# Kernel optimization log

Measured on AMD Instinct MI355X. Metric: run time of the kernel, lower is better.

Reference implementation:

```python
import jax, jax.numpy as jnp
import numpy as np

DIM = 2560
N_HEAD = 32
HEAD_DIM = 80
ROT_DIM = 32  # head_dim * partial_rotary_factor
INTER = 10240
EPS = 1e-5
BASE = 10000.0


def setup_inputs() -> dict:
    key = jax.random.key(0)
    ks = jax.random.split(key, 12)
    B, S, D, I = 1, 2048, DIM, INTER
    s = lambda k, shape, scale: (jax.random.normal(k, shape, jnp.float32) * scale)
    return {
        "x": s(ks[0], (B, S, D), 1.0),
        "input_pos": jnp.arange(S, dtype=jnp.int32),
        "mask": jnp.tril(jnp.ones((S, S), dtype=bool)),
        "ln_w": jnp.ones((D,), jnp.float32),
        "ln_b": jnp.zeros((D,), jnp.float32),
        "wqkv_w": s(ks[1], (3 * D, D), 0.02),
        "wqkv_b": jnp.zeros((3 * D,), jnp.float32),
        "wo_w": s(ks[2], (D, D), 0.02),
        "wo_b": jnp.zeros((D,), jnp.float32),
        "w1_w": s(ks[3], (I, D), 0.02),
        "w1_b": jnp.zeros((I,), jnp.float32),
        "w2_w": s(ks[4], (D, I), 0.02),
        "w2_b": jnp.zeros((D,), jnp.float32),
    }


def _rope_cos_sin(positions):
    # positions: [S] int; returns cos,sin of shape [S, ROT_DIM]
    inv_freq = 1.0 / (BASE ** (jnp.arange(0, ROT_DIM, 2, dtype=jnp.float32) / ROT_DIM))
    freqs = positions.astype(jnp.float32)[:, None] * inv_freq[None, :]  # [S, ROT/2]
    emb = jnp.concatenate([freqs, freqs], axis=-1)  # [S, ROT]
    return jnp.cos(emb), jnp.sin(emb)


def _rotate_half(t):
    t1, t2 = jnp.split(t, 2, axis=-1)
    return jnp.concatenate([-t2, t1], axis=-1)


def _apply_rope(t, cos, sin):
    # t: [B,H,S,hd]; rotary applied to first ROT_DIM dims (partial rotary)
    t_rot, t_pass = t[..., :ROT_DIM], t[..., ROT_DIM:]
    t_rot = t_rot * cos[None, None] + _rotate_half(t_rot) * sin[None, None]
    return jnp.concatenate([t_rot, t_pass], axis=-1)


def reference(x, input_pos, mask, ln_w, ln_b, wqkv_w, wqkv_b, wo_w, wo_b,
              w1_w, w1_b, w2_w, w2_b):
    B, S, D = x.shape
    H, hd = N_HEAD, HEAD_DIM
    # shared LayerNorm (parallel block)
    mu = jnp.mean(x, axis=-1, keepdims=True)
    var = jnp.mean(jnp.square(x - mu), axis=-1, keepdims=True)
    h = (x - mu) * jax.lax.rsqrt(var + EPS) * ln_w + ln_b

    # fused QKV
    qkv = h @ wqkv_w.T + wqkv_b  # [B,S,3D]
    q, k, v = jnp.split(qkv, 3, axis=-1)
    q = q.reshape(B, S, H, hd).transpose(0, 2, 1, 3)  # [B,H,S,hd]
    k = k.reshape(B, S, H, hd).transpose(0, 2, 1, 3)
    v = v.reshape(B, S, H, hd).transpose(0, 2, 1, 3)

    cos, sin = _rope_cos_sin(input_pos)
    q = _apply_rope(q, cos, sin)
    k = _apply_rope(k, cos, sin)

    # causal attention
    scores = jnp.einsum("bhqd,bhkd->bhqk", q, k) / np.sqrt(hd).astype(np.float32)
    scores = jnp.where(mask[None, None], scores, jnp.float32(-1e9))
    attn = jax.nn.softmax(scores, axis=-1)
    y = jnp.einsum("bhqk,bhkd->bhqd", attn, v)  # [B,H,S,hd]
    y = y.transpose(0, 2, 1, 3).reshape(B, S, D)
    attn_out = y @ wo_w.T + wo_b

    # fused MLP (phi2: gelu_new / tanh approx)
    ffn = jax.nn.gelu(h @ w1_w.T + w1_b, approximate=True) @ w2_w.T + w2_b

    return attn_out + ffn + x
```

## Files before the change

kernel.cpp:

```cpp
#include <hip/hip_runtime.h>
#include <cstdint>

#define S_LEN 2048
#define DMODEL 2560
#define NHEADS 32
#define HDIM 80
#define DINTER 10240

typedef unsigned short u16;
typedef __bf16 bf16x8 __attribute__((ext_vector_type(8)));
typedef float f32x4 __attribute__((ext_vector_type(4)));

__device__ __forceinline__ float us2f(u16 u) {
  return __builtin_bit_cast(float, ((uint32_t)u) << 16);
}
__device__ __forceinline__ u16 f2us(float f) {
  uint32_t x = __builtin_bit_cast(uint32_t, f);
  x += 0x7fffu + ((x >> 16) & 1u);
  return (u16)(x >> 16);
}

typedef __attribute__((address_space(1))) void gas_void;
typedef __attribute__((address_space(3))) void las_void;
__device__ __forceinline__ void gld16(const void* g, void* l) {
  __builtin_amdgcn_global_load_lds((gas_void*)g, (las_void*)l, 16, 0, 0);
}

#define VMW(N) asm volatile("s_waitcnt vmcnt(" #N ")" ::: "memory")
#define BARRIER()                          \
  do {                                     \
    asm volatile("" ::: "memory");         \
    __builtin_amdgcn_s_barrier();          \
    asm volatile("" ::: "memory");         \
  } while (0)

__global__ void f2b_kernel(const float* __restrict__ src, u16* __restrict__ dst) {
  const size_t i = ((size_t)blockIdx.x * 256 + threadIdx.x) * 8;
  const float4 a = *(const float4*)(src + i);
  const float4 b = *(const float4*)(src + i + 4);
  u16 o[8] = {f2us(a.x), f2us(a.y), f2us(a.z), f2us(a.w),
              f2us(b.x), f2us(b.y), f2us(b.z), f2us(b.w)};
  *(uint4*)(dst + i) = *(uint4*)o;
}

__global__ void initout_kernel(const float* __restrict__ x,
                               const float* __restrict__ wo_b,
                               const float* __restrict__ w2_b,
                               float* __restrict__ out) {
  const size_t idx = ((size_t)blockIdx.x * 256 + threadIdx.x) * 4;
  const int c0 = (int)(idx % DMODEL);
  const float4 vx = *(const float4*)(x + idx);
  const float4 b1 = *(const float4*)(wo_b + c0);
  const float4 b2 = *(const float4*)(w2_b + c0);
  float4 vo;
  vo.x = vx.x + b1.x + b2.x;
  vo.y = vx.y + b1.y + b2.y;
  vo.z = vx.z + b1.z + b2.z;
  vo.w = vx.w + b1.w + b2.w;
  *(float4*)(out + idx) = vo;
}

__global__ void ln_kernel(const float* __restrict__ x, const float* __restrict__ w,
                          const float* __restrict__ b, u16* __restrict__ h) {
  const int s = blockIdx.x, tid = threadIdx.x;
  const float* xr = x + (size_t)s * DMODEL;
  float v[10];
  float sum = 0.f, sq = 0.f;
#pragma unroll
  for (int j = 0; j < 10; j++) {
    v[j] = xr[tid + j * 256];
    sum += v[j];
    sq += v[j] * v[j];
  }
#pragma unroll
  for (int o = 32; o > 0; o >>= 1) {
    sum += __shfl_down(sum, o, 64);
    sq += __shfl_down(sq, o, 64);
  }
  __shared__ float red[8];
  const int wave = tid >> 6, lane = tid & 63;
  if (lane == 0) { red[wave] = sum; red[4 + wave] = sq; }
  __syncthreads();
  sum = red[0] + red[1] + red[2] + red[3];
  sq = red[4] + red[5] + red[6] + red[7];
  const float mu = sum * (1.0f / DMODEL);
  const float var = sq * (1.0f / DMODEL) - mu * mu;
  const float rstd = rsqrtf(var + 1e-5f);
  u16* hr = h + (size_t)s * DMODEL;
#pragma unroll
  for (int j = 0; j < 10; j++) {
    const int d = tid + j * 256;
    hr[d] = f2us((v[j] - mu) * rstd * w[d] + b[d]);
  }
}

template <int ACT, int MODE>
__launch_bounds__(512, 2)
__global__ void gemm256(const u16* __restrict__ A, const u16* __restrict__ B,
                        const float* __restrict__ bias, void* __restrict__ Cv,
                        int M, int N, int K) {
  __shared__ __align__(16) u16 lds[4][16384];
  const int tid = threadIdx.x;
  const int w = tid >> 6, lane = tid & 63;
  const int quad = lane >> 4, l15 = lane & 15;
  const int wm = w >> 2, wn = w & 3;

  const int nwg = gridDim.x * gridDim.y;
  const int flat = blockIdx.x + gridDim.x * blockIdx.y;
  const int swz = (flat & 7) * (nwg >> 3) + (flat >> 3);
  const int ntN = N >> 8;
  const int bm = swz / ntN, bn = swz % ntN;

  const int Kc = K / gridDim.z;
  const int k0 = Kc * blockIdx.z;
  const int nt = Kc >> 6;

  const int stgCol = (((lane & 7) ^ ((lane >> 3) & 7)) * 8);
  const u16* Ag = A + ((size_t)bm * 256 + w * 8 + (lane >> 3)) * K + k0 + stgCol;
  const u16* Bg = B + ((size_t)bn * 256 + w * 8 + (lane >> 3)) * K + k0 + stgCol;

  const int q8 = quad * 8;
  const int swz3 = (l15 & 7) * 8;
  const int arow = wm * 64 + l15;
  const int brow = wn * 32 + l15;

#define STG_HALF(MAT, GP, BUF, HF, KT)                                       \
  do {                                                                       \
    gld16((GP) + (size_t)((HF) * 128) * K + (size_t)(KT) * 64,               \
          &lds[(BUF) * 2 + (MAT)][(HF) * 8192 + w * 512]);                   \
    gld16((GP) + (size_t)((HF) * 128 + 64) * K + (size_t)(KT) * 64,          \
          &lds[(BUF) * 2 + (MAT)][(HF) * 8192 + 4096 + w * 512]);            \
  } while (0)

#define LDS_A(DST, BUF, MH)                                                  \
  _Pragma("unroll") for (int mf_ = 0; mf_ < 4; mf_++)                        \
  _Pragma("unroll") for (int kk_ = 0; kk_ < 2; kk_++)                        \
      DST[mf_][kk_] = *(const bf16x8*)&lds[(BUF) * 2]                        \
          [(arow + (MH) * 128 + mf_ * 16) * 64 + ((kk_ * 32 + q8) ^ swz3)];

#define LDS_B(DST, BUF, NH)                                                  \
  _Pragma("unroll") for (int nf_ = 0; nf_ < 2; nf_++)                        \
  _Pragma("unroll") for (int kk_ = 0; kk_ < 2; kk_++)                        \
      DST[nf_][kk_] = *(const bf16x8*)&lds[(BUF) * 2 + 1]                    \
          [(brow + (NH) * 128 + nf_ * 16) * 64 + ((kk_ * 32 + q8) ^ swz3)];

#define MFMA_C(MH, NH, AF, BF)                                               \
  do {                                                                       \
    __builtin_amdgcn_s_setprio(1);                                           \
    _Pragma("unroll") for (int kk_ = 0; kk_ < 2; kk_++)                      \
    _Pragma("unroll") for (int mf_ = 0; mf_ < 4; mf_++)                      \
    _Pragma("unroll") for (int nf_ = 0; nf_ < 2; nf_++)                      \
        acc[(MH) * 4 + mf_][(NH) * 2 + nf_] =                                \
            __builtin_amdgcn_mfma_f32_16x16x32_bf16(                         \
                AF[mf_][kk_], BF[nf_][kk_],                                  \
                acc[(MH) * 4 + mf_][(NH) * 2 + nf_], 0, 0, 0);               \
    __builtin_amdgcn_s_setprio(0);                                           \
  } while (0)

  f32x4 acc[8][4] = {};
  bf16x8 aH0[4][2], aH1[4][2], bH0[2][2], bH1[2][2];

  STG_HALF(0, Ag, 0, 0, 0);
  STG_HALF(1, Bg, 0, 0, 0);
  STG_HALF(1, Bg, 0, 1, 0);
  STG_HALF(0, Ag, 0, 1, 0);
  VMW(4);
  BARRIER();
  LDS_A(aH0, 0, 0);
  LDS_B(bH0, 0, 0);

  for (int t = 0; t < nt; ++t) {
    const int bc = t & 1, ob = bc ^ 1;
    const bool more = (t + 1 < nt);
    VMW(0);
    BARRIER();
    if (more) {
      STG_HALF(0, Ag, ob, 0, t + 1);
      STG_HALF(1, Bg, ob, 0, t + 1);
    }
    LDS_B(bH1, bc, 1);
    MFMA_C(0, 0, aH0, bH0);
    if (more) STG_HALF(1, Bg, ob, 1, t + 1);
    LDS_A(aH1, bc, 1);
    MFMA_C(0, 1, aH0, bH1);
    if (more) STG_HALF(0, Ag, ob, 1, t + 1);
    MFMA_C(1, 1, aH1, bH1);
    VMW(4);
    BARRIER();
    MFMA_C(1, 0, aH1, bH0);
    if (more) {
      LDS_A(aH0, ob, 0);
      LDS_B(bH0, ob, 0);
    }
  }

#pragma unroll
  for (int nh = 0; nh < 2; nh++)
#pragma unroll
    for (int nf = 0; nf < 2; nf++) {
      const int col = bn * 256 + nh * 128 + wn * 32 + nf * 16 + l15;
      const float bv = (MODE == 0) ? bias[col] : 0.f;
#pragma unroll
      for (int mh = 0; mh < 2; mh++)
#pragma unroll
        for (int mf = 0; mf < 4; mf++) {
          const int row0 = bm * 256 + mh * 128 + wm * 64 + mf * 16 + quad * 4;
#pragma unroll
          for (int r = 0; r < 4; r++) {
            float v = acc[mh * 4 + mf][nh * 2 + nf][r] + bv;
            if (ACT == 1) {
              const float tt = v * (0.7978845608f + 0.0356774081f * v * v);
              v = 0.5f * v * (1.0f + tanhf(tt));
            }
            if (MODE == 0)
              ((u16*)Cv)[(size_t)(row0 + r) * N + col] = f2us(v);
            else
              atomicAdd((float*)Cv + (size_t)(row0 + r) * N + col, v);
          }
        }
    }
#undef STG_HALF
#undef LDS_A
#undef LDS_B
#undef MFMA_C
}

__global__ void rope_kernel(u16* __restrict__ qkv, const int* __restrict__ pos) {
  const int idx = blockIdx.x * 256 + threadIdx.x;
  const int i = idx & 15;
  const int which = (idx >> 4) & 1;
  const int hh = (idx >> 5) & 31;
  const int s = idx >> 10;
  const float p = (float)pos[s];
  const float freq = p * expf(-0.57564627324851f * (float)i);
  float sn, c;
  sincosf(freq, &sn, &c);
  u16* base = qkv + (size_t)s * (3 * DMODEL) + which * DMODEL + hh * HDIM + i;
  const float t0 = us2f(base[0]), t1 = us2f(base[16]);
  base[0] = f2us(t0 * c - t1 * sn);
  base[16] = f2us(t1 * c + t0 * sn);
}

__global__ void attn_kernel(const u16* __restrict__ qkv, u16* __restrict__ y) {
  const int qt = (int)gridDim.x - 1 - (int)blockIdx.x;
  const int h = blockIdx.y;
  const int tid = threadIdx.x, wave = tid >> 6, lane = tid & 63;
  const int quad = lane >> 4, l15 = lane & 15;
  const int qbase = qt * 64;

  __shared__ __align__(16) u16 Qs[64 * 104];
  __shared__ __align__(16) u16 Ks[64 * 104];
  __shared__ __align__(16) u16 Vts[80 * 88];
  __shared__ __align__(16) u16 Ps[4][2][16 * 40];

  for (int i = tid; i < 64 * 104; i += 256) { Qs[i] = 0; Ks[i] = 0; }
  __syncthreads();

  {
    const int r = tid >> 2, c = tid & 3;
    const u16* src = qkv + (size_t)(qbase + r) * (3 * DMODEL) + h * HDIM + c * 20;
    u16* dst = Qs + r * 104 + c * 20;
#pragma unroll
    for (int j = 0; j < 5; j++) {
      ushort4 uv = *(const ushort4*)(src + j * 4);
      ushort4 ov;
      ov.x = f2us(us2f(uv.x) * 0.11180339887f);
      ov.y = f2us(us2f(uv.y) * 0.11180339887f);
      ov.z = f2us(us2f(uv.z) * 0.11180339887f);
      ov.w = f2us(us2f(uv.w) * 0.11180339887f);
      *(ushort4*)(dst + j * 4) = ov;
    }
  }

  float m_i[4], l_i[4];
  f32x4 oacc[5] = {};
#pragma unroll
  for (int r = 0; r < 4; r++) { m_i[r] = -1e30f; l_i[r] = 0.f; }

  const int n_iter = qt + 1;
  __syncthreads();

  for (int it = 0; it < n_iter; ++it) {
    const int kc0 = it * 64;
    if (tid < 128) {
      const int r = tid >> 1, c = (tid & 1) * 40;
      const u16* src =
          qkv + (size_t)(kc0 + r) * (3 * DMODEL) + DMODEL + h * HDIM + c;
      u16* dst = Ks + r * 104 + c;
#pragma unroll
      for (int j = 0; j < 10; j++)
        *(ushort4*)(dst + j * 4) = *(const ushort4*)(src + j * 4);
    } else {
      const int u = tid - 128;
      const int r = u >> 1, c0 = (u & 1) * 40;
      const u16* src =
          qkv + (size_t)(kc0 + r) * (3 * DMODEL) + 2 * DMODEL + h * HDIM + c0;
#pragma unroll
      for (int j = 0; j < 10; j++) {
        ushort4 vv = *(const ushort4*)(src + j * 4);
        const int d0 = c0 + j * 4;
        Vts[(d0 + 0) * 88 + r] = vv.x;
        Vts[(d0 + 1) * 88 + r] = vv.y;
        Vts[(d0 + 2) * 88 + r] = vv.z;
        Vts[(d0 + 3) * 88 + r] = vv.w;
      }
    }
    __syncthreads();

    f32x4 st[4] = {};
    bf16x8 aq[3];
#pragma unroll
    for (int ks = 0; ks < 3; ks++)
      aq[ks] = *(const bf16x8*)&Qs[(wave * 16 + l15) * 104 + ks * 32 + quad * 8];
#pragma unroll
    for (int ks = 0; ks < 3; ks++)
#pragma unroll
      for (int t = 0; t < 4; t++) {
        bf16x8 bk = *(const bf16x8*)&Ks[(t * 16 + l15) * 104 + ks * 32 + quad * 8];
        st[t] = __builtin_amdgcn_mfma_f32_16x16x32_bf16(aq[ks], bk, st[t], 0, 0, 0);
      }

    float sv[4][4], mx[4];
#pragma unroll
    for (int r = 0; r < 4; r++) {
      const int qr = qbase + wave * 16 + quad * 4 + r;
#pragma unroll
      for (int t = 0; t < 4; t++) {
        const int kc = kc0 + t * 16 + l15;
        sv[t][r] = (kc <= qr) ? st[t][r] : -1e30f;
      }
      mx[r] = fmaxf(fmaxf(sv[0][r], sv[1][r]), fmaxf(sv[2][r], sv[3][r]));
    }
#pragma unroll
    for (int o = 1; o < 16; o <<= 1)
#pragma unroll
      for (int r = 0; r < 4; r++) mx[r] = fmaxf(mx[r], __shfl_xor(mx[r], o, 64));

    float alpha[4], rs[4];
#pragma unroll
    for (int r = 0; r < 4; r++) {
      const float mnew = fmaxf(m_i[r], mx[r]);
      alpha[r] = __expf(m_i[r] - mnew);
      m_i[r] = mnew;
      const float p0 = __expf(sv[0][r] - mnew);
      const float p1 = __expf(sv[1][r] - mnew);
      const float p2 = __expf(sv[2][r] - mnew);
      const float p3 = __expf(sv[3][r] - mnew);
      rs[r] = (p0 + p1) + (p2 + p3);
      const int ro = (quad * 4 + r) * 40;
      Ps[wave][0][ro + l15] = f2us(p0);
      Ps[wave][0][ro + 16 + l15] = f2us(p1);
      Ps[wave][1][ro + l15] = f2us(p2);
      Ps[wave][1][ro + 16 + l15] = f2us(p3);
    }
#pragma unroll
    for (int o = 1; o < 16; o <<= 1)
#pragma unroll
      for (int r = 0; r < 4; r++) rs[r] += __shfl_xor(rs[r], o, 64);
#pragma unroll
    for (int r = 0; r < 4; r++) l_i[r] = l_i[r] * alpha[r] + rs[r];
#pragma unroll
    for (int dt = 0; dt < 5; dt++)
#pragma unroll
      for (int r = 0; r < 4; r++) oacc[dt][r] *= alpha[r];

    bf16x8 pf0 = *(const bf16x8*)&Ps[wave][0][l15 * 40 + quad * 8];
    bf16x8 pf1 = *(const bf16x8*)&Ps[wave][1][l15 * 40 + quad * 8];
#pragma unroll
    for (int dt = 0; dt < 5; dt++) {
      bf16x8 vf0 = *(const bf16x8*)&Vts[(dt * 16 + l15) * 88 + quad * 8];
      bf16x8 vf1 = *(const bf16x8*)&Vts[(dt * 16 + l15) * 88 + 32 + quad * 8];
      oacc[dt] = __builtin_amdgcn_mfma_f32_16x16x32_bf16(pf0, vf0, oacc[dt], 0, 0, 0);
      oacc[dt] = __builtin_amdgcn_mfma_f32_16x16x32_bf16(pf1, vf1, oacc[dt], 0, 0, 0);
    }
    __syncthreads();
  }

#pragma unroll
  for (int dt = 0; dt < 5; dt++)
#pragma unroll
    for (int r = 0; r < 4; r++) {
      const int row = qbase + wave * 16 + quad * 4 + r;
      y[(size_t)row * DMODEL + h * HDIM + dt * 16 + l15] = f2us(oacc[dt][r] / l_i[r]);
    }
}

extern "C" void kernel_launch(void* const* d_in, const int* in_sizes, int n_in,
                              void* d_out, int out_size, void* d_ws, size_t ws_size,
                              hipStream_t stream) {
  const float* x = (const float*)d_in[0];
  const int* pos = (const int*)d_in[1];
  const float* ln_w = (const float*)d_in[3];
  const float* ln_b = (const float*)d_in[4];
  const float* wqkv_w = (const float*)d_in[5];
  const float* wqkv_b = (const float*)d_in[6];
  const float* wo_w = (const float*)d_in[7];
  const float* wo_b = (const float*)d_in[8];
  const float* w1_w = (const float*)d_in[9];
  const float* w1_b = (const float*)d_in[10];
  const float* w2_w = (const float*)d_in[11];
  const float* w2_b = (const float*)d_in[12];
  float* out = (float*)d_out;

  char* ws = (char*)d_ws;
  u16* wbuf = (u16*)(ws);
  u16* h = (u16*)(ws + 52428800);
  u16* ffn1 = (u16*)(ws + 62914560);
  u16* qkv = (u16*)(ws + 62914560);
  u16* yAtt = (u16*)(ws + 94371840);

  ln_kernel<<<S_LEN, 256, 0, stream>>>(x, ln_w, ln_b, h);
  initout_kernel<<<(S_LEN * DMODEL / 4) / 256, 256, 0, stream>>>(x, wo_b, w2_b, out);

  f2b_kernel<<<(DINTER * DMODEL) / 2048, 256, 0, stream>>>(w1_w, wbuf);
  gemm256<1, 0><<<dim3(DINTER / 256, S_LEN / 256, 1), 512, 0, stream>>>(
      h, wbuf, w1_b, ffn1, S_LEN, DINTER, DMODEL);
  f2b_kernel<<<(DMODEL * DINTER) / 2048, 256, 0, stream>>>(w2_w, wbuf);
  gemm256<0, 2><<<dim3(DMODEL / 256, S_LEN / 256, 5), 512, 0, stream>>>(
      ffn1, wbuf, w2_b, out, S_LEN, DMODEL, DINTER);

  f2b_kernel<<<(3 * DMODEL * DMODEL) / 2048, 256, 0, stream>>>(wqkv_w, wbuf);
  gemm256<0, 0><<<dim3(3 * DMODEL / 256, S_LEN / 256, 1), 512, 0, stream>>>(
      h, wbuf, wqkv_b, qkv, S_LEN, 3 * DMODEL, DMODEL);
  rope_kernel<<<(S_LEN * NHEADS * 2 * 16) / 256, 256, 0, stream>>>(qkv, pos);
  attn_kernel<<<dim3(S_LEN / 64, NHEADS), 256, 0, stream>>>(qkv, yAtt);
  f2b_kernel<<<(DMODEL * DMODEL) / 2048, 256, 0, stream>>>(wo_w, wbuf);
  gemm256<0, 2><<<dim3(DMODEL / 256, S_LEN / 256, 2), 512, 0, stream>>>(
      yAtt, wbuf, wo_b, out, S_LEN, DMODEL, DMODEL);
}
```

Before: 976.0 us.

## Double-buffer K/V tiles in attention with register prefetch and packed V transpose

The attention kernel now keeps two shared-memory buffers for K and transposed V. The next tile's global loads go into registers before the current tile's MFMA work and are written to the other buffer afterwards, which removes one barrier per iteration and hides load latency. The V transpose now packs two rows into 32-bit stores instead of scattered 16-bit stores. Q fragments are hoisted out of the loop, causal masking runs only on the diagonal tile, and zero-init covers only the padding columns. In exchange it uses more LDS and registers, which may lower occupancy.

```diff
diff --git a/kernel.cpp b/kernel.cpp
--- a/kernel.cpp
+++ b/kernel.cpp
@@ -249,12 +249,22 @@
   const int qbase = qt * 64;
 
   __shared__ __align__(16) u16 Qs[64 * 104];
-  __shared__ __align__(16) u16 Ks[64 * 104];
-  __shared__ __align__(16) u16 Vts[80 * 88];
+  __shared__ __align__(16) u16 Ks[2][64 * 104];
+  __shared__ __align__(16) u16 Vts[2][80 * 88];
   __shared__ __align__(16) u16 Ps[4][2][16 * 40];
 
-  for (int i = tid; i < 64 * 104; i += 256) { Qs[i] = 0; Ks[i] = 0; }
-  __syncthreads();
+  if (tid < 128) {
+    const int b = tid >> 6, r = tid & 63;
+    u16* z = &Ks[b][r * 104 + 80];
+    *(uint4*)z = uint4{0, 0, 0, 0};
+    *(uint4*)(z + 8) = uint4{0, 0, 0, 0};
+  } else if (tid < 192) {
+    const int r = tid & 63;
+    u16* z = &Qs[r * 104 + 80];
+    *(uint4*)z = uint4{0, 0, 0, 0};
+    *(uint4*)(z + 8) = uint4{0, 0, 0, 0};
+    *(uint4*)(z + 16) = uint4{0, 0, 0, 0};
+  }
 
   {
     const int r = tid >> 2, c = tid & 3;
@@ -272,65 +282,97 @@
     }
   }
 
+  {
+    const int r = tid >> 2, c4 = (tid & 3) * 20;
+    const u16* sK = qkv + (size_t)r * (3 * DMODEL) + DMODEL + h * HDIM + c4;
+    u16* dK = &Ks[0][r * 104 + c4];
+#pragma unroll
+    for (int j = 0; j < 5; j++) *(uint2*)(dK + j * 4) = *(const uint2*)(sK + j * 4);
+  }
+  if (tid < 160) {
+    const int p = tid & 31, cc = tid >> 5;
+    const u16* sV = qkv + (size_t)(2 * p) * (3 * DMODEL) + 2 * DMODEL + h * HDIM + cc * 16;
+    const uint4 a0 = *(const uint4*)sV;
+    const uint4 b0 = *(const uint4*)(sV + 8);
+    const uint4 a1 = *(const uint4*)(sV + 3 * DMODEL);
+    const uint4 b1 = *(const uint4*)(sV + 3 * DMODEL + 8);
+    const uint32_t A0[8] = {a0.x, a0.y, a0.z, a0.w, b0.x, b0.y, b0.z, b0.w};
+    const uint32_t A1[8] = {a1.x, a1.y, a1.z, a1.w, b1.x, b1.y, b1.z, b1.w};
+    uint32_t* dV = (uint32_t*)Vts[0];
+#pragma unroll
+    for (int d = 0; d < 16; d++) {
+      const int j = d >> 1, s = (d & 1) * 16;
+      const uint32_t o = ((A0[j] >> s) & 0xffffu) | (((A1[j] >> s) & 0xffffu) << 16);
+      dV[(cc * 16 + d) * 44 + p] = o;
+    }
+  }
+
   float m_i[4], l_i[4];
   f32x4 oacc[5] = {};
 #pragma unroll
   for (int r = 0; r < 4; r++) { m_i[r] = -1e30f; l_i[r] = 0.f; }
 
+  __syncthreads();
+
+  bf16x8 aq[3];
+#pragma unroll
+  for (int ks = 0; ks < 3; ks++)
+    aq[ks] = *(const bf16x8*)&Qs[(wave * 16 + l15) * 104 + ks * 32 + quad * 8];
+
   const int n_iter = qt + 1;
-  __syncthreads();
+  uint2 kr[5];
+  uint4 v0a = {}, v0b = {}, v1a = {}, v1b = {};
 
   for (int it = 0; it < n_iter; ++it) {
+    const int cur = it & 1;
+    const bool more = (it + 1 < n_iter);
+    if (more) {
+      const int kcn = (it + 1) * 64;
+      const int r = tid >> 2, c4 = (tid & 3) * 20;
+      const u16* sK = qkv + (size_t)(kcn + r) * (3 * DMODEL) + DMODEL + h * HDIM + c4;
+#pragma unroll
+      for (int j = 0; j < 5; j++) kr[j] = *(const uint2*)(sK + j * 4);
+      if (tid < 160) {
+        const int p = tid & 31, cc = tid >> 5;
+        const u16* sV =
+            qkv + (size_t)(kcn + 2 * p) * (3 * DMODEL) + 2 * DMODEL + h * HDIM + cc * 16;
+        v0a = *(const uint4*)sV;
+        v0b = *(const uint4*)(sV + 8);
+        v1a = *(const uint4*)(sV + 3 * DMODEL);
+        v1b = *(const uint4*)(sV + 3 * DMODEL + 8);
+      }
+    }
+
     const int kc0 = it * 64;
-    if (tid < 128) {
-      const int r = tid >> 1, c = (tid & 1) * 40;
-      const u16* src =
-          qkv + (size_t)(kc0 + r) * (3 * DMODEL) + DMODEL + h * HDIM + c;
-      u16* dst = Ks + r * 104 + c;
-#pragma unroll
-      for (int j = 0; j < 10; j++)
-        *(ushort4*)(dst + j * 4) = *(const ushort4*)(src + j * 4);
-    } else {
-      const int u = tid - 128;
-      const int r = u >> 1, c0 = (u & 1) * 40;
-      const u16* src =
-          qkv + (size_t)(kc0 + r) * (3 * DMODEL) + 2 * DMODEL + h * HDIM + c0;
-#pragma unroll
-      for (int j = 0; j < 10; j++) {
-        ushort4 vv = *(const ushort4*)(src + j * 4);
-        const int d0 = c0 + j * 4;
-        Vts[(d0 + 0) * 88 + r] = vv.x;
-        Vts[(d0 + 1) * 88 + r] = vv.y;
-        Vts[(d0 + 2) * 88 + r] = vv.z;
-        Vts[(d0 + 3) * 88 + r] = vv.w;
-      }
-    }
-    __syncthreads();
-
     f32x4 st[4] = {};
-    bf16x8 aq[3];
 #pragma unroll
     for (int ks = 0; ks < 3; ks++)
-      aq[ks] = *(const bf16x8*)&Qs[(wave * 16 + l15) * 104 + ks * 32 + quad * 8];
-#pragma unroll
-    for (int ks = 0; ks < 3; ks++)
 #pragma unroll
       for (int t = 0; t < 4; t++) {
-        bf16x8 bk = *(const bf16x8*)&Ks[(t * 16 + l15) * 104 + ks * 32 + quad * 8];
+        bf16x8 bk = *(const bf16x8*)&Ks[cur][(t * 16 + l15) * 104 + ks * 32 + quad * 8];
         st[t] = __builtin_amdgcn_mfma_f32_16x16x32_bf16(aq[ks], bk, st[t], 0, 0, 0);
       }
 
     float sv[4][4], mx[4];
-#pragma unroll
-    for (int r = 0; r < 4; r++) {
-      const int qr = qbase + wave * 16 + quad * 4 + r;
-#pragma unroll
-      for (int t = 0; t < 4; t++) {
-        const int kc = kc0 + t * 16 + l15;
-        sv[t][r] = (kc <= qr) ? st[t][r] : -1e30f;
+    if (it == qt) {
+#pragma unroll
+      for (int r = 0; r < 4; r++) {
+        const int qr = qbase + wave * 16 + quad * 4 + r;
+#pragma unroll
+        for (int t = 0; t < 4; t++) {
+          const int kc = kc0 + t * 16 + l15;
+          sv[t][r] = (kc <= qr) ? st[t][r] : -1e30f;
+        }
       }
+    } else {
+#pragma unroll
+      for (int r = 0; r < 4; r++)
+#pragma unroll
+        for (int t = 0; t < 4; t++) sv[t][r] = st[t][r];
+    }
+#pragma unroll
+    for (int r = 0; r < 4; r++)
       mx[r] = fmaxf(fmaxf(sv[0][r], sv[1][r]), fmaxf(sv[2][r], sv[3][r]));
-    }
 #pragma unroll
     for (int o = 1; o < 16; o <<= 1)
 #pragma unroll
@@ -368,10 +410,32 @@
     bf16x8 pf1 = *(const bf16x8*)&Ps[wave][1][l15 * 40 + quad * 8];
 #pragma unroll
     for (int dt = 0; dt < 5; dt++) {
-      bf16x8 vf0 = *(const bf16x8*)&Vts[(dt * 16 + l15) * 88 + quad * 8];
-      bf16x8 vf1 = *(const bf16x8*)&Vts[(dt * 16 + l15) * 88 + 32 + quad * 8];
+      bf16x8 vf0 = *(const bf16x8*)&Vts[cur][(dt * 16 + l15) * 88 + quad * 8];
+      bf16x8 vf1 = *(const bf16x8*)&Vts[cur][(dt * 16 + l15) * 88 + 32 + quad * 8];
       oacc[dt] = __builtin_amdgcn_mfma_f32_16x16x32_bf16(pf0, vf0, oacc[dt], 0, 0, 0);
       oacc[dt] = __builtin_amdgcn_mfma_f32_16x16x32_bf16(pf1, vf1, oacc[dt], 0, 0, 0);
+    }
+
+    if (more) {
+      const int r = tid >> 2, c4 = (tid & 3) * 20;
+      u16* dK = &Ks[cur ^ 1][r * 104 + c4];
+#pragma unroll
+      for (int j = 0; j < 5; j++) *(uint2*)(dK + j * 4) = kr[j];
+      if (tid < 160) {
+        const int p = tid & 31, cc = tid >> 5;
+        const uint32_t A0[8] = {v0a.x, v0a.y, v0a.z, v0a.w,
+                                v0b.x, v0b.y, v0b.z, v0b.w};
+        const uint32_t A1[8] = {v1a.x, v1a.y, v1a.z, v1a.w,
+                                v1b.x, v1b.y, v1b.z, v1b.w};
+        uint32_t* dV = (uint32_t*)Vts[cur ^ 1];
+#pragma unroll
+        for (int d = 0; d < 16; d++) {
+          const int j = d >> 1, s = (d & 1) * 16;
+          const uint32_t o =
+              ((A0[j] >> s) & 0xffffu) | (((A1[j] >> s) & 0xffffu) << 16);
+          dV[(cc * 16 + d) * 44 + p] = o;
+        }
+      }
     }
     __syncthreads();
   }
```

Result: no change. 959.6 us (-1.7%).
